# Kernel optimization log

Hardware: AMD Instinct MI355X
Metric: run time of the kernel (lower is better)

Reference implementation:

```python
import jax, jax.numpy as jnp
import numpy as np
from jax import lax

K = 5          # kernel_size
OC = 8         # out_num_capsules
OD = 32        # out_dims


def setup_inputs() -> dict:
    key = jax.random.key(0)
    k1, k2, k3 = jax.random.split(key, 3)
    u = jax.random.normal(k1, (4, 4, 16, 128, 128), jnp.float32)            # [B, in_caps, in_dims, H, W]
    W = jax.random.normal(k2, (4, OC * OD, 16, K, K), jnp.float32) * 0.05    # per-capsule Conv2d weights (OIHW)
    bias = jax.random.normal(k3, (4, OC * OD), jnp.float32) * 0.05
    return {"u": u, "W": W, "bias": bias}


def _squash(p):
    # p: [..., out_dims]
    sq = jnp.sum(p * p, axis=-1, keepdims=True)
    return sq / (1.0 + sq) * p / jnp.sqrt(sq + 1e-9)


def reference(u, W, bias):
    B, ic, _, H, Wd = u.shape

    def conv_one(x, w, b):  # x:[B,in_dims,H,W] w:[OC*OD,in_dims,K,K]
        y = lax.conv_general_dilated(x, w, (1, 1), [(2, 2), (2, 2)],
                                     dimension_numbers=("NCHW", "OIHW", "NCHW"))
        return y + b[None, :, None, None]

    # per-capsule conv, vmapped over the in_capsule axis -> [B, ic, OC*OD, H, W]
    u_hat = jax.vmap(conv_one, in_axes=(1, 0, 0), out_axes=1)(u, W, bias)
    # -> [B, ic, H, W, OC, OD] (matches torch reshape + transpose_(1,3).transpose_(2,4))
    u_hat = u_hat.reshape(B, ic, OC, OD, H, Wd).transpose(0, 1, 4, 5, 2, 3)

    # Routing logits b start at zero. NOTE: in the source, the update `b_t_list_`
    # is a dead store (never assigned back), so b stays zero for all iterations
    # and every routing iteration produces the identical v; one effective pass.
    b_r = jnp.zeros((B, OC, H, Wd), u.dtype)
    # windowed max (torch max_pool2d pads with -inf; k=5, pad=2 == SAME)
    b_max = lax.reduce_window(b_r, -jnp.inf, lax.max, (1, 1, K, K), (1, 1, 1, 1), "SAME")
    b_max = jnp.max(b_max, axis=1, keepdims=True)                 # [B,1,H,W]
    c = jnp.exp(b_r - b_max)                                      # [B,OC,H,W]
    # conv2d_same with an all-ones (1, OC, K, K) kernel == channel-sum then SAME window-sum
    sum_c = lax.reduce_window(jnp.sum(c, axis=1, keepdims=True), 0.0, lax.add,
                              (1, 1, K, K), (1, 1, 1, 1), "SAME")  # [B,1,H,W]
    r = (c / sum_c).transpose(0, 2, 3, 1)[..., None]              # [B,H,W,OC,1]

    # r is identical for every input capsule (b==0), so fold the capsule sum
    p = jnp.sum(r[:, None] * u_hat, axis=1)                       # [B,H,W,OC,OD]
    v = _squash(p)
    # final v.transpose_(1,3).transpose_(2,4) -> [B, OC, OD, H, W]
    return v.transpose(0, 3, 4, 1, 2)
```

## Files before the change

### kernel.cpp

```cpp
#include <hip/hip_runtime.h>
#include <math.h>

typedef __attribute__((ext_vector_type(8))) __bf16 b16x8;
typedef __attribute__((ext_vector_type(4))) float f32x4;

__device__ __forceinline__ unsigned short f2bf(float x) {
    unsigned int v = __float_as_uint(x);
    v += 0x7fffu + ((v >> 16) & 1u);
    return (unsigned short)(v >> 16);
}

__global__ __launch_bounds__(256) void repack_w(
    const float* __restrict__ Wt, const float* __restrict__ bias,
    unsigned short* __restrict__ wsw, float* __restrict__ wsb) {
    int idx = blockIdx.x * 256 + threadIdx.x;
    if (idx < 409600) {
        int j    = idx & 7;
        int lane = (idx >> 3) & 63;
        int fr   = (idx >> 9) & 1;
        int wn   = (idx >> 10) & 7;
        int l    = idx >> 13;
        int kh   = l % 5;
        int ks   = (l / 5) & 1;
        int kw   = l / 10;
        int tap  = kh * 5 + kw;
        int col  = lane & 15;
        int cg   = lane >> 4;
        int o    = wn * 32 + fr * 16 + col;
        int cin  = ks * 32 + cg * 8 + j;
        int ic = cin >> 4, id = cin & 15;
        float w = Wt[((size_t)(ic * 256 + o) * 16 + id) * 25 + tap];
        wsw[idx] = f2bf(w);
    } else if (idx < 409856) {
        int o = idx - 409600;
        float s = 0.f;
        for (int ic = 0; ic < 4; ++ic) s += bias[ic * 256 + o];
        wsb[o] = s;
    }
}

__global__ __launch_bounds__(1024, 4) void caps_mfma(
    const float* __restrict__ u, const unsigned short* __restrict__ wsw,
    const float* __restrict__ wsb, float* __restrict__ out) {

    __shared__ __align__(16) unsigned short su_sh[25600];

    const int tid  = threadIdx.x;
    const int lane = tid & 63;
    const int wid  = tid >> 6;
    const int wm   = wid >> 3;
    const int wn   = wid & 7;
    const int col  = lane & 15;
    const int xg   = lane >> 4;
    const int ybase = wm * 8;

    const int bx  = blockIdx.x;
    const int b   = blockIdx.y;
    const int ty0 = (bx >> 3) * 16;
    const int tx0 = (bx & 7) * 16;

    f32x4 acc[8][2];
    #pragma unroll
    for (int f = 0; f < 8; ++f) {
        acc[f][0] = (f32x4)0.f;
        acc[f][1] = (f32x4)0.f;
    }

    auto stage_u = [&](int half) {
        const float* up = u + ((size_t)b * 64 + half * 32) * 16384;
        unsigned short* dstp = su_sh + half * 12800;
        #pragma unroll 1
        for (int i = tid; i < 12800; i += 1024) {
            int c = i / 400;
            int s = i - c * 400;
            int hy = s / 20, hx = s - hy * 20;
            int gy = ty0 - 2 + hy, gx = tx0 - 2 + hx;
            float v = 0.f;
            if ((unsigned)gy < 128u && (unsigned)gx < 128u)
                v = up[(size_t)c * 16384 + gy * 128 + gx];
            int cgp = (c >> 3) ^ ((hx >> 1) & 3);
            dstp[(hy * 20 + hx) * 32 + cgp * 8 + (c & 7)] = f2bf(v);
        }
    };

    const char* wp0 = ((const char*)wsw) + wn * 2048 + lane * 16;

    b16x8 bf[3][2];
    #define LOADB(SLOT, BUF)                                                   \
        {                                                                      \
            const char* p_ = wp0 + (size_t)((SLOT) > 49 ? 49 : (SLOT)) * 16384;\
            bf[BUF][0] = *reinterpret_cast<const b16x8*>(p_);                  \
            bf[BUF][1] = *reinterpret_cast<const b16x8*>(p_ + 1024);           \
        }

    LOADB(0, 0)
    LOADB(1, 1)
    stage_u(0);
    stage_u(1);
    __syncthreads();

    #pragma unroll
    for (int g = 0; g < 5; ++g) {
        const int hx   = col + g;
        const int coff = hx * 32 + ((xg ^ ((hx >> 1) & 3)) * 8);
        #pragma unroll
        for (int ks = 0; ks < 2; ++ks) {
            const unsigned short* apb =
                su_sh + ks * 12800 + ybase * 640 + coff;

            b16x8 aw[8];
            #pragma unroll
            for (int i = 0; i < 8; ++i)
                aw[i] = *reinterpret_cast<const b16x8*>(apb + i * 640);

            #pragma unroll
            for (int kh = 0; kh < 5; ++kh) {
                const int l = g * 10 + ks * 5 + kh;

                LOADB(l + 2, (l + 2) % 3)

                __builtin_amdgcn_s_setprio(1);
                #pragma unroll
                for (int f = 0; f < 8; ++f) {
                    acc[f][0] = __builtin_amdgcn_mfma_f32_16x16x32_bf16(
                        bf[l % 3][0], aw[(kh + f) & 7], acc[f][0], 0, 0, 0);
                    acc[f][1] = __builtin_amdgcn_mfma_f32_16x16x32_bf16(
                        bf[l % 3][1], aw[(kh + f) & 7], acc[f][1], 0, 0, 0);
                }
                __builtin_amdgcn_s_setprio(0);

                if (kh < 4)
                    aw[kh & 7] = *reinterpret_cast<const b16x8*>(
                        apb + (kh + 8) * 640);
            }
        }
    }
    #undef LOADB

    float4 bb0 = *reinterpret_cast<const float4*>(wsb + wn * 32 + xg * 4);
    float4 bb1 = *reinterpret_cast<const float4*>(wsb + wn * 32 + 16 + xg * 4);

    const int x = tx0 + col;
    const int colsv = min(x + 2, 127) - max(x - 2, 0) + 1;
    float* pout = out + ((size_t)(b * 8 + wn) * 32 + xg * 4) * 16384 + x;

    #pragma unroll
    for (int f = 0; f < 8; ++f) {
        int h = ty0 + ybase + f;
        int rows = min(h + 2, 127) - max(h - 2, 0) + 1;
        float rs = 1.0f / (8.0f * (float)(rows * colsv));
        float p[8];
        float sq = 0.f;
        #pragma unroll
        for (int r = 0; r < 4; ++r) {
            float v0 = (acc[f][0][r] + bb0[r]) * rs;
            float v1 = (acc[f][1][r] + bb1[r]) * rs;
            p[r] = v0; p[4 + r] = v1;
            sq += v0 * v0;
            sq += v1 * v1;
        }
        sq += __shfl_xor(sq, 16);
        sq += __shfl_xor(sq, 32);
        float scale = sq / ((1.0f + sq) * sqrtf(sq + 1e-9f));
        float* ph = pout + (size_t)h * 128;
        #pragma unroll
        for (int r = 0; r < 4; ++r) {
            ph[(size_t)r * 16384]        = p[r] * scale;
            ph[(size_t)(16 + r) * 16384] = p[4 + r] * scale;
        }
    }
}

extern "C" void kernel_launch(void* const* d_in, const int* in_sizes, int n_in,
                              void* d_out, int out_size, void* d_ws, size_t ws_size,
                              hipStream_t stream) {
    const float* u    = (const float*)d_in[0];
    const float* Wt   = (const float*)d_in[1];
    const float* bias = (const float*)d_in[2];
    unsigned short* wsw = (unsigned short*)d_ws;
    float* wsb = (float*)((char*)d_ws + 819200);

    repack_w<<<1601, 256, 0, stream>>>(Wt, bias, wsw, wsb);
    caps_mfma<<<dim3(64, 4), 1024, 0, stream>>>(u, wsw, wsb, (float*)d_out);
}
```

Before: 59.06 us.

## Switch conv MFMA from 16x16x32 to 32x32x16 bf16 tiles

```diff
diff --git a/kernel.cpp b/kernel.cpp
--- a/kernel.cpp
+++ b/kernel.cpp
@@ -2,7 +2,7 @@
 #include <math.h>
 
 typedef __attribute__((ext_vector_type(8))) __bf16 b16x8;
-typedef __attribute__((ext_vector_type(4))) float f32x4;
+typedef __attribute__((ext_vector_type(16))) float f32x16;
 
 __device__ __forceinline__ unsigned short f2bf(float x) {
     unsigned int v = __float_as_uint(x);
@@ -17,17 +17,15 @@
     if (idx < 409600) {
         int j    = idx & 7;
         int lane = (idx >> 3) & 63;
-        int fr   = (idx >> 9) & 1;
+        int kseg = (idx >> 9) & 1;
         int wn   = (idx >> 10) & 7;
         int l    = idx >> 13;
         int kh   = l % 5;
         int ks   = (l / 5) & 1;
         int kw   = l / 10;
         int tap  = kh * 5 + kw;
-        int col  = lane & 15;
-        int cg   = lane >> 4;
-        int o    = wn * 32 + fr * 16 + col;
-        int cin  = ks * 32 + cg * 8 + j;
+        int o    = wn * 32 + (lane & 31);
+        int cin  = ks * 32 + kseg * 16 + (lane >> 5) * 8 + j;
         int ic = cin >> 4, id = cin & 15;
         float w = Wt[((size_t)(ic * 256 + o) * 16 + id) * 25 + tap];
         wsw[idx] = f2bf(w);
@@ -50,21 +48,20 @@
     const int wid  = tid >> 6;
     const int wm   = wid >> 3;
     const int wn   = wid & 7;
-    const int col  = lane & 15;
-    const int xg   = lane >> 4;
+    const int n31  = lane & 31;
+    const int hi   = lane >> 5;
+    const int xl   = n31 & 15;
     const int ybase = wm * 8;
+    const int ybw  = ybase + (n31 >> 4) * 4;
 
     const int bx  = blockIdx.x;
     const int b   = blockIdx.y;
     const int ty0 = (bx >> 3) * 16;
     const int tx0 = (bx & 7) * 16;
 
-    f32x4 acc[8][2];
+    f32x16 acc[4];
     #pragma unroll
-    for (int f = 0; f < 8; ++f) {
-        acc[f][0] = (f32x4)0.f;
-        acc[f][1] = (f32x4)0.f;
-    }
+    for (int t = 0; t < 4; ++t) acc[t] = (f32x16)0.f;
 
     auto stage_u = [&](int half) {
         const float* up = u + ((size_t)b * 64 + half * 32) * 16384;
@@ -85,89 +82,97 @@
 
     const char* wp0 = ((const char*)wsw) + wn * 2048 + lane * 16;
 
-    b16x8 bf[3][2];
-    #define LOADB(SLOT, BUF)                                                   \
+    b16x8 wf[3][2];
+    #define LOADA(SLOT, BUF)                                                   \
         {                                                                      \
             const char* p_ = wp0 + (size_t)((SLOT) > 49 ? 49 : (SLOT)) * 16384;\
-            bf[BUF][0] = *reinterpret_cast<const b16x8*>(p_);                  \
-            bf[BUF][1] = *reinterpret_cast<const b16x8*>(p_ + 1024);           \
+            wf[BUF][0] = *reinterpret_cast<const b16x8*>(p_);                  \
+            wf[BUF][1] = *reinterpret_cast<const b16x8*>(p_ + 1024);           \
         }
 
-    LOADB(0, 0)
-    LOADB(1, 1)
+    LOADA(0, 0)
+    LOADA(1, 1)
     stage_u(0);
     stage_u(1);
     __syncthreads();
 
     #pragma unroll
     for (int g = 0; g < 5; ++g) {
-        const int hx   = col + g;
-        const int coff = hx * 32 + ((xg ^ ((hx >> 1) & 3)) * 8);
+        const int hxl  = xl + g;
+        const int xorb = (hxl >> 1) & 3;
+        const int off0 = ybw * 640 + hxl * 32 + ((hi ^ xorb) * 8);
+        const int off1 = ybw * 640 + hxl * 32 + (((2 + hi) ^ xorb) * 8);
         #pragma unroll
         for (int ks = 0; ks < 2; ++ks) {
-            const unsigned short* apb =
-                su_sh + ks * 12800 + ybase * 640 + coff;
+            const unsigned short* base0 = su_sh + ks * 12800 + off0;
+            const unsigned short* base1 = su_sh + ks * 12800 + off1;
 
-            b16x8 aw[8];
+            b16x8 aw0[4], aw1[4];
             #pragma unroll
-            for (int i = 0; i < 8; ++i)
-                aw[i] = *reinterpret_cast<const b16x8*>(apb + i * 640);
+            for (int i = 0; i < 4; ++i) {
+                aw0[i] = *reinterpret_cast<const b16x8*>(base0 + i * 640);
+                aw1[i] = *reinterpret_cast<const b16x8*>(base1 + i * 640);
+            }
 
             #pragma unroll
             for (int kh = 0; kh < 5; ++kh) {
                 const int l = g * 10 + ks * 5 + kh;
 
-                LOADB(l + 2, (l + 2) % 3)
+                LOADA(l + 2, (l + 2) % 3)
 
                 __builtin_amdgcn_s_setprio(1);
                 #pragma unroll
-                for (int f = 0; f < 8; ++f) {
-                    acc[f][0] = __builtin_amdgcn_mfma_f32_16x16x32_bf16(
-                        bf[l % 3][0], aw[(kh + f) & 7], acc[f][0], 0, 0, 0);
-                    acc[f][1] = __builtin_amdgcn_mfma_f32_16x16x32_bf16(
-                        bf[l % 3][1], aw[(kh + f) & 7], acc[f][1], 0, 0, 0);
+                for (int t = 0; t < 4; ++t) {
+                    acc[t] = __builtin_amdgcn_mfma_f32_32x32x16_bf16(
+                        wf[l % 3][0], aw0[(kh + t) & 3], acc[t], 0, 0, 0);
+                    acc[t] = __builtin_amdgcn_mfma_f32_32x32x16_bf16(
+                        wf[l % 3][1], aw1[(kh + t) & 3], acc[t], 0, 0, 0);
                 }
                 __builtin_amdgcn_s_setprio(0);
 
-                if (kh < 4)
-                    aw[kh & 7] = *reinterpret_cast<const b16x8*>(
-                        apb + (kh + 8) * 640);
+                if (kh < 4) {
+                    aw0[kh & 3] = *reinterpret_cast<const b16x8*>(
+                        base0 + (kh + 4) * 640);
+                    aw1[kh & 3] = *reinterpret_cast<const b16x8*>(
+                        base1 + (kh + 4) * 640);
+                }
             }
         }
     }
-    #undef LOADB
+    #undef LOADA
 
-    float4 bb0 = *reinterpret_cast<const float4*>(wsb + wn * 32 + xg * 4);
-    float4 bb1 = *reinterpret_cast<const float4*>(wsb + wn * 32 + 16 + xg * 4);
+    float4 bb[4];
+    #pragma unroll
+    for (int q = 0; q < 4; ++q)
+        bb[q] = *reinterpret_cast<const float4*>(wsb + wn * 32 + q * 8 + hi * 4);
 
-    const int x = tx0 + col;
+    const int x = tx0 + xl;
     const int colsv = min(x + 2, 127) - max(x - 2, 0) + 1;
-    float* pout = out + ((size_t)(b * 8 + wn) * 32 + xg * 4) * 16384 + x;
+    float* pout = out + ((size_t)(b * 8 + wn) * 32 + 4 * hi) * 16384 + x;
 
     #pragma unroll
-    for (int f = 0; f < 8; ++f) {
-        int h = ty0 + ybase + f;
-        int rows = min(h + 2, 127) - max(h - 2, 0) + 1;
+    for (int t = 0; t < 4; ++t) {
+        int y = ty0 + ybw + t;
+        int rows = min(y + 2, 127) - max(y - 2, 0) + 1;
         float rs = 1.0f / (8.0f * (float)(rows * colsv));
-        float p[8];
+        float p[16];
         float sq = 0.f;
         #pragma unroll
-        for (int r = 0; r < 4; ++r) {
-            float v0 = (acc[f][0][r] + bb0[r]) * rs;
-            float v1 = (acc[f][1][r] + bb1[r]) * rs;
-            p[r] = v0; p[4 + r] = v1;
-            sq += v0 * v0;
-            sq += v1 * v1;
-        }
-        sq += __shfl_xor(sq, 16);
+        for (int q = 0; q < 4; ++q)
+            #pragma unroll
+            for (int r = 0; r < 4; ++r) {
+                float v = (acc[t][q * 4 + r] + bb[q][r]) * rs;
+                p[q * 4 + r] = v;
+                sq += v * v;
+            }
         sq += __shfl_xor(sq, 32);
         float scale = sq / ((1.0f + sq) * sqrtf(sq + 1e-9f));
-        float* ph = pout + (size_t)h * 128;
+        float* ph = pout + (size_t)y * 128;
         #pragma unroll
-        for (int r = 0; r < 4; ++r) {
-            ph[(size_t)r * 16384]        = p[r] * scale;
-            ph[(size_t)(16 + r) * 16384] = p[4 + r] * scale;
-        }
+        for (int q = 0; q < 4; ++q)
+            #pragma unroll
+            for (int r = 0; r < 4; ++r)
+                ph[(size_t)(q * 8 + r) * 16384] = p[q * 4 + r] * scale;
     }
 }
 
```

Measured after the change: 69.82 us. +18.2%, slower.
